# Kernel tuning notes

Hardware: AMD Instinct MI355X
Metric: run time of the kernel (lower is better)

Reference implementation:

```python
import jax, jax.numpy as jnp
import numpy as np

GROUPS = [[0, 1, 2, 3, 4], [5, 7, 9], [6, 8, 10], [11, 13, 15], [12, 14, 16]]
G = len(GROUPS)
BN_EPS = 1e-5


def _fc_edges(n):
    r = np.repeat(np.arange(n), n)
    c = np.tile(np.arange(n), n)
    m = r != c
    return jnp.asarray(r[m]), jnp.asarray(c[m])


ROW, COL = _fc_edges(G)  # [E], E = G*(G-1) = 20


def _bn(x, scale, bias, mean, var):
    # inference-mode batchnorm over last dim
    return (x - mean) * (scale * jax.lax.rsqrt(var + BN_EPS)) + bias


def setup_inputs() -> dict:
    key = jax.random.key(0)
    ks = jax.random.split(key, 12)
    B, K, C, Ci = 4096, 17, 256, 64
    inp = {
        "x_bk_c": jax.random.normal(ks[0], (B * K, C), jnp.float32),
        "W_down": jax.random.normal(ks[1], (C, Ci), jnp.float32) * 0.05,
        "b_down": jax.random.normal(ks[2], (Ci,), jnp.float32) * 0.05,
        "bn1_scale": jax.random.uniform(ks[3], (Ci,), jnp.float32, 0.5, 1.5),
        "bn1_bias": jax.random.normal(ks[4], (Ci,), jnp.float32) * 0.1,
        "bn1_mean": jax.random.normal(ks[5], (Ci,), jnp.float32) * 0.1,
        "bn1_var": jax.random.uniform(ks[6], (Ci,), jnp.float32, 0.5, 1.5),
        "W_conv": jax.random.normal(ks[7], (Ci, 2 * Ci), jnp.float32) * 0.05,  # 1x1 conv, bias=False
        "bn2_scale": jax.random.uniform(ks[8], (Ci,), jnp.float32, 0.5, 1.5),
        "bn2_bias": jax.random.normal(ks[9], (Ci,), jnp.float32) * 0.1,
        "bn2_mean": jax.random.normal(ks[10], (Ci,), jnp.float32) * 0.1,
        "bn2_var": jax.random.uniform(ks[11], (Ci,), jnp.float32, 0.5, 1.5),
        "W_agg": jax.random.normal(jax.random.fold_in(key, 100), (Ci, C), jnp.float32) * 0.05,
        "b_agg": jax.random.normal(jax.random.fold_in(key, 101), (C,), jnp.float32) * 0.05,
        "B": B,
        "K": K,
    }
    return inp


def reference(x_bk_c, W_down, b_down, bn1_scale, bn1_bias, bn1_mean, bn1_var,
              W_conv, bn2_scale, bn2_bias, bn2_mean, bn2_var, W_agg, b_agg, B, K):
    C = x_bk_c.shape[-1]
    # down-projection + BN + SiLU
    xd = jax.nn.silu(_bn(x_bk_c @ W_down + b_down, bn1_scale, bn1_bias, bn1_mean, bn1_var))
    xd = xd.reshape(B, K, -1)  # [B, K, Ci]
    # per-group mean pooling (static small loop over 5 groups)
    means = jnp.stack([xd[:, g, :].mean(axis=1) for g in GROUPS], axis=1)  # [B, G, Ci]
    # EdgeConv over fully-connected group graph
    x_i = means[:, ROW, :]                                   # [B, E, Ci]
    x_j = means[:, COL, :]
    ef = jnp.concatenate([x_i, x_j - x_i], axis=-1)          # [B, E, 2Ci]
    pe = jax.nn.silu(_bn(ef @ W_conv.T, bn2_scale, bn2_bias, bn2_mean, bn2_var))  # [B, E, Ci]
    agg = jnp.zeros_like(means).at[:, ROW, :].add(pe)        # scatter-add over target nodes
    # per-group attention scores in C_in
    att = jax.nn.sigmoid(agg @ W_agg + b_agg)                # [B, G, C]
    # average group scores over each keypoint's memberships
    M = np.zeros((K, G), np.float32)
    for gi, g in enumerate(GROUPS):
        for kp in g:
            M[kp, gi] += 1.0
    Mj = jnp.asarray(M)
    cnt = Mj.sum(axis=1, keepdims=True)                      # [K, 1]
    ssum = jnp.einsum('kg,bgc->bkc', Mj, att)                # [B, K, C]
    safe = jnp.where(cnt > 0, cnt, 1.0)
    final = jnp.where(cnt > 0, ssum / safe, 1.0)             # ungrouped kps -> 1.0
    return (x_bk_c.reshape(B, K, C) * final).reshape(B * K, C)
```

## Files before the change

kernel.cpp:

```cpp
#include <hip/hip_runtime.h>

typedef float  v4f    __attribute__((ext_vector_type(4)));
typedef float  f32x4  __attribute__((ext_vector_type(4)));
typedef short  bf16x8 __attribute__((ext_vector_type(8)));

namespace {
constexpr int XBSTR = 264;
constexpr int XDT   = 24;
constexpr int MWC   = 129;
constexpr int ATS   = 258;
constexpr int MSTR  = 72;
constexpr int FRAG_SLOTS = 5120;

__device__ __forceinline__ float fsilu(float v){ return v/(1.f+__expf(-v)); }
__device__ __forceinline__ float fsigm(float v){ return 1.f/(1.f+__expf(-v)); }

__device__ __forceinline__ unsigned f2bf2(float a, float b){
  unsigned r;
  asm("v_cvt_pk_bf16_f32 %0, %1, %2" : "=v"(r) : "v"(a), "v"(b));
  return r;
}
__device__ __forceinline__ short f2bf(float f){
  unsigned u = __builtin_bit_cast(unsigned, f);
  return (short)((u + 0x7FFFu + ((u>>16)&1u)) >> 16);
}
__device__ __forceinline__ float bf2f(short s){
  unsigned u = ((unsigned)(unsigned short)s) << 16;
  return __builtin_bit_cast(float, u);
}

template<bool USE_WS>
__device__ __forceinline__ bf16x8 get_bd(const bf16x8* wsf, const float* Wd,
                                         int nt, int ks, int l){
  if constexpr (USE_WS) return wsf[(nt*8 + ks)*64 + l];
  bf16x8 f;
  #pragma unroll
  for (int j = 0; j < 8; ++j) f[j] = f2bf(Wd[(ks*32 + (l>>4)*8 + j)*64 + nt*16 + (l&15)]);
  return f;
}
template<bool USE_WS>
__device__ __forceinline__ bf16x8 get_bc(const bf16x8* wsf, const float* Wc,
                                         int nt, int ks, int l){
  if constexpr (USE_WS) return wsf[2048 + (nt*2 + ks)*64 + l];
  const int col = nt*16 + (l&15), cw = col>>6, co = col&63;
  bf16x8 f;
  #pragma unroll
  for (int j = 0; j < 8; ++j) f[j] = f2bf(Wc[co*128 + cw*64 + ks*32 + (l>>4)*8 + j]);
  return f;
}
template<bool USE_WS>
__device__ __forceinline__ bf16x8 get_ba(const bf16x8* wsf, const float* Wa,
                                         int nt, int ks, int l){
  if constexpr (USE_WS) return wsf[3072 + (nt*2 + ks)*64 + l];
  const int col = nt*16 + (l&15);
  bf16x8 f;
  #pragma unroll
  for (int j = 0; j < 8; ++j) f[j] = f2bf(Wa[(ks*32 + (l>>4)*8 + j)*256 + col]);
  return f;
}
}

__global__ __launch_bounds__(256)
void pack_frags(const float* __restrict__ Wd, const float* __restrict__ Wc,
                const float* __restrict__ Wa, bf16x8* __restrict__ wsf)
{
  const int e  = blockIdx.x*256 + threadIdx.x;
  const int l  = e & 63;
  const int fi = e >> 6;
  bf16x8 f;
  if (fi < 32) {
    const int nt = fi >> 3, ks = fi & 7;
    #pragma unroll
    for (int j = 0; j < 8; ++j) f[j] = f2bf(Wd[(ks*32 + (l>>4)*8 + j)*64 + nt*16 + (l&15)]);
  } else if (fi < 48) {
    const int idx = fi - 32, nt = idx >> 1, ks = idx & 1;
    const int col = nt*16 + (l&15), cw = col>>6, co = col&63;
    #pragma unroll
    for (int j = 0; j < 8; ++j) f[j] = f2bf(Wc[co*128 + cw*64 + ks*32 + (l>>4)*8 + j]);
  } else {
    const int idx = fi - 48, nt = idx >> 1, ks = idx & 1;
    const int col = nt*16 + (l&15);
    #pragma unroll
    for (int j = 0; j < 8; ++j) f[j] = f2bf(Wa[(ks*32 + (l>>4)*8 + j)*256 + col]);
  }
  wsf[e] = f;
}

template<bool USE_WS>
__global__ __launch_bounds__(256, 8)
void fused_gnn_v9(const float* __restrict__ x,
                  const float* __restrict__ Wd, const float* __restrict__ bd,
                  const float* __restrict__ bn1s, const float* __restrict__ bn1b,
                  const float* __restrict__ bn1m, const float* __restrict__ bn1v,
                  const float* __restrict__ Wc,
                  const float* __restrict__ bn2s, const float* __restrict__ bn2b,
                  const float* __restrict__ bn2m, const float* __restrict__ bn2v,
                  const float* __restrict__ Wa, const float* __restrict__ ba,
                  const bf16x8* __restrict__ wsf,
                  float* __restrict__ out)
{
  __shared__ short xbf[18*XBSTR];
  __shared__ __align__(16) char uni_raw[3072];
  __shared__ float mw[5*MWC];
  __shared__ short mbf[16*MSTR];
  __shared__ short abf[16*MSTR];

  short* xdT = (short*)uni_raw;
  short* att = (short*)uni_raw;

  const int tid  = threadIdx.x;
  const int l    = tid & 63;
  const int wv   = tid >> 6;
  const int arow = l & 15;
  const int ak8  = (l >> 4) * 8;
  const int b    = blockIdx.x;
  const int colA = wv*16 + arow;

  const float a1r = bn1s[colA] * rsqrtf(bn1v[colA] + 1e-5f);
  const float b1r = (bd[colA] - bn1m[colA])*a1r + bn1b[colA];
  const float a2r = bn2s[l] * rsqrtf(bn2v[l] + 1e-5f);
  const float b2r = bn2b[l] - bn2m[l]*a2r;

  {
    const v4f* x4 = (const v4f*)(x + (size_t)b * 4352);
    #pragma unroll
    for (int i = 0; i < 5; ++i) {
      const int idx = i*256 + tid;
      if (idx < 1088) {
        const v4f v = x4[idx];
        const int r = idx >> 6, c4 = (idx & 63) * 4;
        uint2 u; u.x = f2bf2(v.x, v.y); u.y = f2bf2(v.z, v.w);
        *(uint2*)&xbf[r*XBSTR + c4] = u;
      }
    }
  }
  __syncthreads();

  {
    f32x4 acc0 = {0.f,0.f,0.f,0.f};
    f32x4 acc1 = {0.f,0.f,0.f,0.f};
    const int rowT = (arow == 0) ? 16 : 17;
    #pragma unroll
    for (int h = 0; h < 2; ++h) {
      bf16x8 Bd[4];
      #pragma unroll
      for (int k4 = 0; k4 < 4; ++k4) Bd[k4] = get_bd<USE_WS>(wsf, Wd, wv, h*4 + k4, l);
      #pragma unroll
      for (int k4 = 0; k4 < 4; ++k4) {
        const int ks = h*4 + k4;
        bf16x8 a0 = *(const bf16x8*)&xbf[arow*XBSTR + ks*32 + ak8];
        acc0 = __builtin_amdgcn_mfma_f32_16x16x32_bf16(a0, Bd[k4], acc0, 0, 0, 0);
        bf16x8 a1 = *(const bf16x8*)&xbf[rowT*XBSTR + ks*32 + ak8];
        acc1 = __builtin_amdgcn_mfma_f32_16x16x32_bf16(a1, Bd[k4], acc1, 0, 0, 0);
      }
    }
    const float s0 = fsilu(acc0[0]*a1r + b1r);
    const float s1 = fsilu(acc0[1]*a1r + b1r);
    const float s2 = fsilu(acc0[2]*a1r + b1r);
    const float s3 = fsilu(acc0[3]*a1r + b1r);
    uint2 u; u.x = f2bf2(s0, s1); u.y = f2bf2(s2, s3);
    *(uint2*)&xdT[colA*XDT + (l>>4)*4] = u;
    if ((l >> 4) == 0)
      xdT[colA*XDT + 16] = f2bf(fsilu(acc1[0]*a1r + b1r));
  }
  __syncthreads();

  {
    const bf16x8 rA = *(const bf16x8*)&xdT[l*XDT];
    const bf16x8 rB = *(const bf16x8*)&xdT[l*XDT + 8];
    const float x16 = bf2f(xdT[l*XDT + 16]);
    float xv[16];
    #pragma unroll
    for (int k = 0; k < 8; ++k) { xv[k] = bf2f(rA[k]); xv[k+8] = bf2f(rB[k]); }
    const float m0 = (xv[0]+xv[1]+xv[2]+xv[3]+xv[4])*0.2f;
    const float m1 = (xv[5]+xv[7]+xv[9])*(1.f/3.f);
    const float m2 = (xv[6]+xv[8]+xv[10])*(1.f/3.f);
    const float m3 = (xv[11]+xv[13]+xv[15])*(1.f/3.f);
    const float m4 = (xv[12]+xv[14]+x16)*(1.f/3.f);
    unsigned p01 = f2bf2(m0, m1);
    unsigned p23 = f2bf2(m2, m3);
    mbf[0*MSTR + l] = (short)(p01 & 0xFFFFu);
    mbf[1*MSTR + l] = (short)(p01 >> 16);
    mbf[2*MSTR + l] = (short)(p23 & 0xFFFFu);
    mbf[3*MSTR + l] = (short)(p23 >> 16);
    mbf[4*MSTR + l] = f2bf(m4);
  }

  {
    bf16x8 am[2];
    #pragma unroll
    for (int ks = 0; ks < 2; ++ks)
      am[ks] = *(const bf16x8*)&mbf[arow*MSTR + ks*32 + ak8];
    #pragma unroll
    for (int t = 0; t < 2; ++t) {
      const int nt = wv*2 + t;
      f32x4 acc = {0.f,0.f,0.f,0.f};
      #pragma unroll
      for (int ks = 0; ks < 2; ++ks)
        acc = __builtin_amdgcn_mfma_f32_16x16x32_bf16(
                am[ks], get_bc<USE_WS>(wsf, Wc, nt, ks, l), acc, 0, 0, 0);
      #pragma unroll
      for (int j = 0; j < 4; ++j) {
        const int g = (l>>4)*4 + j;
        if (g < 5) mw[g*MWC + nt*16 + arow] = acc[j];
      }
    }
  }
  __syncthreads();

  {
    float m2c[5];
    #pragma unroll
    for (int cc = 0; cc < 5; ++cc) m2c[cc] = mw[cc*MWC + 64 + l];
    #pragma unroll
    for (int g = 0; g < 5; ++g) {
      const float bse = mw[g*MWC + l] - m2c[g];
      float s = 0.f;
      #pragma unroll
      for (int cc = 0; cc < 5; ++cc) {
        if (cc != g) s += fsilu((bse + m2c[cc])*a2r + b2r);
      }
      abf[g*MSTR + l] = f2bf(s);
    }
  }

  {
    bf16x8 ae[2];
    #pragma unroll
    for (int ks = 0; ks < 2; ++ks)
      ae[ks] = *(const bf16x8*)&abf[arow*MSTR + ks*32 + ak8];
    #pragma unroll
    for (int t = 0; t < 4; ++t) {
      const int nt = wv*4 + t;
      const int colE = nt*16 + arow;
      f32x4 acc = {0.f,0.f,0.f,0.f};
      #pragma unroll
      for (int ks = 0; ks < 2; ++ks)
        acc = __builtin_amdgcn_mfma_f32_16x16x32_bf16(
                ae[ks], get_ba<USE_WS>(wsf, Wa, nt, ks, l), acc, 0, 0, 0);
      const float bav = ba[colE];
      #pragma unroll
      for (int j = 0; j < 4; ++j) {
        const int g = (l>>4)*4 + j;
        if (g < 5) att[g*ATS + colE] = f2bf(fsigm(acc[j] + bav));
      }
    }
  }
  __syncthreads();

  {
    const int c = tid;
    float a5[5];
    #pragma unroll
    for (int g = 0; g < 5; ++g) a5[g] = bf2f(att[g*ATS + c]);
    float* og = out + (size_t)b*4352 + c;
    constexpr int GOF[17] = {0,0,0,0,0,1,2,1,2,1,2,3,4,3,4,3,4};
    #pragma unroll
    for (int k = 0; k < 17; ++k)
      og[k*256] = bf2f(xbf[k*XBSTR + c]) * a5[GOF[k]];
  }
}

extern "C" void kernel_launch(void* const* d_in, const int* in_sizes, int n_in,
                              void* d_out, int out_size, void* d_ws, size_t ws_size,
                              hipStream_t stream) {
    (void)n_in; (void)out_size;
    const float* x   = (const float*)d_in[0];
    const float* Wd  = (const float*)d_in[1];
    const float* bd  = (const float*)d_in[2];
    const float* s1  = (const float*)d_in[3];
    const float* b1  = (const float*)d_in[4];
    const float* m1  = (const float*)d_in[5];
    const float* v1  = (const float*)d_in[6];
    const float* Wc  = (const float*)d_in[7];
    const float* s2  = (const float*)d_in[8];
    const float* b2  = (const float*)d_in[9];
    const float* m2  = (const float*)d_in[10];
    const float* v2  = (const float*)d_in[11];
    const float* Wa  = (const float*)d_in[12];
    const float* ba  = (const float*)d_in[13];

    const int Btot = in_sizes[0] / (17 * 256);
    bf16x8* wsf = (bf16x8*)d_ws;

    if (ws_size >= (size_t)FRAG_SLOTS * 16) {
        pack_frags<<<FRAG_SLOTS/256, 256, 0, stream>>>(Wd, Wc, Wa, wsf);
        fused_gnn_v9<true><<<Btot, 256, 0, stream>>>(
            x, Wd, bd, s1, b1, m1, v1, Wc, s2, b2, m2, v2, Wa, ba,
            wsf, (float*)d_out);
    } else {
        fused_gnn_v9<false><<<Btot, 256, 0, stream>>>(
            x, Wd, bd, s1, b1, m1, v1, Wc, s2, b2, m2, v2, Wa, ba,
            wsf, (float*)d_out);
    }
}
```

Baseline: 46.92 us.

## Process one batch item per wavefront, removing block barriers and x staging in LDS

Each wavefront now handles a whole batch item (4 items per block) instead of four waves sharing one item. x is loaded straight into registers as bf16 MFMA fragments rather than staged through shared memory, group means are reduced with cross-lane shuffles, and all __syncthreads are removed because each wave uses private LDS slices. This targets barrier stalls and LDS traffic. In exchange each wave does four times the MFMA and weight-fragment loads, register pressure goes up (launch bounds drop to 4), the grid assumes B is divisible by 4, and output is rebuilt from bf16-rounded x except for row 16.

```diff
diff --git a/kernel.cpp b/kernel.cpp
--- a/kernel.cpp
+++ b/kernel.cpp
@@ -1,15 +1,14 @@
 #include <hip/hip_runtime.h>
 
-typedef float  v4f    __attribute__((ext_vector_type(4)));
-typedef float  f32x4  __attribute__((ext_vector_type(4)));
-typedef short  bf16x8 __attribute__((ext_vector_type(8)));
+typedef float    v4f    __attribute__((ext_vector_type(4)));
+typedef float    f32x4  __attribute__((ext_vector_type(4)));
+typedef short    bf16x8 __attribute__((ext_vector_type(8)));
+typedef unsigned u32x4  __attribute__((ext_vector_type(4)));
 
 namespace {
-constexpr int XBSTR = 264;
-constexpr int XDT   = 24;
-constexpr int MWC   = 129;
-constexpr int ATS   = 258;
-constexpr int MSTR  = 72;
+constexpr int MSTR = 72;
+constexpr int MWC  = 129;
+constexpr int ATS  = 264;
 constexpr int FRAG_SLOTS = 5120;
 
 __device__ __forceinline__ float fsilu(float v){ return v/(1.f+__expf(-v)); }
@@ -27,6 +26,14 @@
 __device__ __forceinline__ float bf2f(short s){
   unsigned u = ((unsigned)(unsigned short)s) << 16;
   return __builtin_bit_cast(float, u);
+}
+__device__ __forceinline__ bf16x8 pack4(unsigned u0, unsigned u1, unsigned u2, unsigned u3){
+  u32x4 u = {u0, u1, u2, u3};
+  return __builtin_bit_cast(bf16x8, u);
+}
+__device__ __forceinline__ bf16x8 cvt8(v4f lo, v4f hi){
+  return pack4(f2bf2(lo.x, lo.y), f2bf2(lo.z, lo.w),
+               f2bf2(hi.x, hi.y), f2bf2(hi.z, hi.w));
 }
 
 template<bool USE_WS>
@@ -87,177 +94,192 @@
 }
 
 template<bool USE_WS>
-__global__ __launch_bounds__(256, 8)
-void fused_gnn_v9(const float* __restrict__ x,
-                  const float* __restrict__ Wd, const float* __restrict__ bd,
-                  const float* __restrict__ bn1s, const float* __restrict__ bn1b,
-                  const float* __restrict__ bn1m, const float* __restrict__ bn1v,
-                  const float* __restrict__ Wc,
-                  const float* __restrict__ bn2s, const float* __restrict__ bn2b,
-                  const float* __restrict__ bn2m, const float* __restrict__ bn2v,
-                  const float* __restrict__ Wa, const float* __restrict__ ba,
-                  const bf16x8* __restrict__ wsf,
-                  float* __restrict__ out)
+__global__ __launch_bounds__(256, 4)
+void fused_gnn_v19(const float* __restrict__ x,
+                   const float* __restrict__ Wd, const float* __restrict__ bd,
+                   const float* __restrict__ bn1s, const float* __restrict__ bn1b,
+                   const float* __restrict__ bn1m, const float* __restrict__ bn1v,
+                   const float* __restrict__ Wc,
+                   const float* __restrict__ bn2s, const float* __restrict__ bn2b,
+                   const float* __restrict__ bn2m, const float* __restrict__ bn2v,
+                   const float* __restrict__ Wa, const float* __restrict__ ba,
+                   const bf16x8* __restrict__ wsf,
+                   float* __restrict__ out)
 {
-  __shared__ short xbf[18*XBSTR];
-  __shared__ __align__(16) char uni_raw[3072];
-  __shared__ float mw[5*MWC];
-  __shared__ short mbf[16*MSTR];
-  __shared__ short abf[16*MSTR];
-
-  short* xdT = (short*)uni_raw;
-  short* att = (short*)uni_raw;
+  __shared__ short mbfs[4][21*MSTR];
+  __shared__ float mws [4][5*MWC];
+  __shared__ short atts[4][5*ATS];
 
   const int tid  = threadIdx.x;
   const int l    = tid & 63;
   const int wv   = tid >> 6;
+  short* mbf = mbfs[wv];
+  short* abf = mbfs[wv] + 5*MSTR;
+  float* mw  = mws[wv];
+  short* att = atts[wv];
+
   const int arow = l & 15;
-  const int ak8  = (l >> 4) * 8;
-  const int b    = blockIdx.x;
-  const int colA = wv*16 + arow;
-
-  const float a1r = bn1s[colA] * rsqrtf(bn1v[colA] + 1e-5f);
-  const float b1r = (bd[colA] - bn1m[colA])*a1r + bn1b[colA];
-  const float a2r = bn2s[l] * rsqrtf(bn2v[l] + 1e-5f);
+  const int q4   = l >> 4;
+  const int ak8  = q4 * 8;
+  const int b    = blockIdx.x*4 + wv;
+  const float* xb = x + (size_t)b * 4352;
+
+  float a1c0, a1c1, a1c2, a1c3, b1c0, b1c1, b1c2, b1c3;
+  {
+    const int c0 = 0*16+arow, c1 = 1*16+arow, c2 = 2*16+arow, c3 = 3*16+arow;
+    a1c0 = bn1s[c0]*rsqrtf(bn1v[c0]+1e-5f); b1c0 = (bd[c0]-bn1m[c0])*a1c0 + bn1b[c0];
+    a1c1 = bn1s[c1]*rsqrtf(bn1v[c1]+1e-5f); b1c1 = (bd[c1]-bn1m[c1])*a1c1 + bn1b[c1];
+    a1c2 = bn1s[c2]*rsqrtf(bn1v[c2]+1e-5f); b1c2 = (bd[c2]-bn1m[c2])*a1c2 + bn1b[c2];
+    a1c3 = bn1s[c3]*rsqrtf(bn1v[c3]+1e-5f); b1c3 = (bd[c3]-bn1m[c3])*a1c3 + bn1b[c3];
+  }
+  const float a2r = bn2s[l]*rsqrtf(bn2v[l]+1e-5f);
   const float b2r = bn2b[l] - bn2m[l]*a2r;
 
-  {
-    const v4f* x4 = (const v4f*)(x + (size_t)b * 4352);
-    #pragma unroll
-    for (int i = 0; i < 5; ++i) {
-      const int idx = i*256 + tid;
-      if (idx < 1088) {
-        const v4f v = x4[idx];
-        const int r = idx >> 6, c4 = (idx & 63) * 4;
-        uint2 u; u.x = f2bf2(v.x, v.y); u.y = f2bf2(v.z, v.w);
-        *(uint2*)&xbf[r*XBSTR + c4] = u;
-      }
-    }
-  }
-  __syncthreads();
-
-  {
+  bf16x8 xf[8];
+  bf16x8 xt[8];
+  {
+    const int rowT = (arow == 0) ? 16 : 0;
+    #pragma unroll
+    for (int ks = 0; ks < 8; ++ks) {
+      v4f lo = *(const v4f*)(xb + arow*256 + ks*32 + ak8);
+      v4f hi = *(const v4f*)(xb + arow*256 + ks*32 + ak8 + 4);
+      xf[ks] = cvt8(lo, hi);
+      v4f tl = *(const v4f*)(xb + rowT*256 + ks*32 + ak8);
+      v4f th = *(const v4f*)(xb + rowT*256 + ks*32 + ak8 + 4);
+      xt[ks] = cvt8(tl, th);
+    }
+  }
+
+  #pragma unroll
+  for (int nt = 0; nt < 4; ++nt) {
+    const float a1v = (nt==0)?a1c0:(nt==1)?a1c1:(nt==2)?a1c2:a1c3;
+    const float b1v = (nt==0)?b1c0:(nt==1)?b1c1:(nt==2)?b1c2:b1c3;
     f32x4 acc0 = {0.f,0.f,0.f,0.f};
     f32x4 acc1 = {0.f,0.f,0.f,0.f};
-    const int rowT = (arow == 0) ? 16 : 17;
     #pragma unroll
     for (int h = 0; h < 2; ++h) {
       bf16x8 Bd[4];
       #pragma unroll
-      for (int k4 = 0; k4 < 4; ++k4) Bd[k4] = get_bd<USE_WS>(wsf, Wd, wv, h*4 + k4, l);
+      for (int k4 = 0; k4 < 4; ++k4) Bd[k4] = get_bd<USE_WS>(wsf, Wd, nt, h*4 + k4, l);
       #pragma unroll
       for (int k4 = 0; k4 < 4; ++k4) {
         const int ks = h*4 + k4;
-        bf16x8 a0 = *(const bf16x8*)&xbf[arow*XBSTR + ks*32 + ak8];
-        acc0 = __builtin_amdgcn_mfma_f32_16x16x32_bf16(a0, Bd[k4], acc0, 0, 0, 0);
-        bf16x8 a1 = *(const bf16x8*)&xbf[rowT*XBSTR + ks*32 + ak8];
-        acc1 = __builtin_amdgcn_mfma_f32_16x16x32_bf16(a1, Bd[k4], acc1, 0, 0, 0);
+        acc0 = __builtin_amdgcn_mfma_f32_16x16x32_bf16(xf[ks], Bd[k4], acc0, 0, 0, 0);
+        acc1 = __builtin_amdgcn_mfma_f32_16x16x32_bf16(xt[ks], Bd[k4], acc1, 0, 0, 0);
       }
     }
-    const float s0 = fsilu(acc0[0]*a1r + b1r);
-    const float s1 = fsilu(acc0[1]*a1r + b1r);
-    const float s2 = fsilu(acc0[2]*a1r + b1r);
-    const float s3 = fsilu(acc0[3]*a1r + b1r);
-    uint2 u; u.x = f2bf2(s0, s1); u.y = f2bf2(s2, s3);
-    *(uint2*)&xdT[colA*XDT + (l>>4)*4] = u;
-    if ((l >> 4) == 0)
-      xdT[colA*XDT + 16] = f2bf(fsilu(acc1[0]*a1r + b1r));
-  }
-  __syncthreads();
-
-  {
-    const bf16x8 rA = *(const bf16x8*)&xdT[l*XDT];
-    const bf16x8 rB = *(const bf16x8*)&xdT[l*XDT + 8];
-    const float x16 = bf2f(xdT[l*XDT + 16]);
-    float xv[16];
-    #pragma unroll
-    for (int k = 0; k < 8; ++k) { xv[k] = bf2f(rA[k]); xv[k+8] = bf2f(rB[k]); }
-    const float m0 = (xv[0]+xv[1]+xv[2]+xv[3]+xv[4])*0.2f;
-    const float m1 = (xv[5]+xv[7]+xv[9])*(1.f/3.f);
-    const float m2 = (xv[6]+xv[8]+xv[10])*(1.f/3.f);
-    const float m3 = (xv[11]+xv[13]+xv[15])*(1.f/3.f);
-    const float m4 = (xv[12]+xv[14]+x16)*(1.f/3.f);
-    unsigned p01 = f2bf2(m0, m1);
-    unsigned p23 = f2bf2(m2, m3);
-    mbf[0*MSTR + l] = (short)(p01 & 0xFFFFu);
-    mbf[1*MSTR + l] = (short)(p01 >> 16);
-    mbf[2*MSTR + l] = (short)(p23 & 0xFFFFu);
-    mbf[3*MSTR + l] = (short)(p23 >> 16);
-    mbf[4*MSTR + l] = f2bf(m4);
-  }
-
-  {
-    bf16x8 am[2];
-    #pragma unroll
-    for (int ks = 0; ks < 2; ++ks)
-      am[ks] = *(const bf16x8*)&mbf[arow*MSTR + ks*32 + ak8];
-    #pragma unroll
-    for (int t = 0; t < 2; ++t) {
-      const int nt = wv*2 + t;
+    const float s0 = fsilu(acc0[0]*a1v + b1v);
+    const float s1 = fsilu(acc0[1]*a1v + b1v);
+    const float s2 = fsilu(acc0[2]*a1v + b1v);
+    const float s3 = fsilu(acc0[3]*a1v + b1v);
+    const float st = fsilu(acc1[0]*a1v + b1v);
+    float p0 = 0.f, p1 = 0.f, p2 = 0.f, p3 = 0.f, p4 = 0.f;
+    if (q4 == 0)      { p0 = s0+s1+s2+s3; p4 = st; }
+    else if (q4 == 1) { p0 = s0; p1 = s1+s3; p2 = s2; }
+    else if (q4 == 2) { p2 = s0+s2; p1 = s1; p3 = s3; }
+    else              { p4 = s0+s2; p3 = s1+s3; }
+    p0 += __shfl_xor(p0, 16); p0 += __shfl_xor(p0, 32);
+    p1 += __shfl_xor(p1, 16); p1 += __shfl_xor(p1, 32);
+    p2 += __shfl_xor(p2, 16); p2 += __shfl_xor(p2, 32);
+    p3 += __shfl_xor(p3, 16); p3 += __shfl_xor(p3, 32);
+    p4 += __shfl_xor(p4, 16); p4 += __shfl_xor(p4, 32);
+    if (q4 == 0) {
+      const int col = nt*16 + arow;
+      mbf[0*MSTR + col] = f2bf(p0 * 0.2f);
+      mbf[1*MSTR + col] = f2bf(p1 * (1.f/3.f));
+      mbf[2*MSTR + col] = f2bf(p2 * (1.f/3.f));
+      mbf[3*MSTR + col] = f2bf(p3 * (1.f/3.f));
+      mbf[4*MSTR + col] = f2bf(p4 * (1.f/3.f));
+    }
+  }
+
+  {
+    const bf16x8 am0 = *(const bf16x8*)&mbf[arow*MSTR + 0*32 + ak8];
+    const bf16x8 am1 = *(const bf16x8*)&mbf[arow*MSTR + 1*32 + ak8];
+    #pragma unroll
+    for (int nt = 0; nt < 8; ++nt) {
       f32x4 acc = {0.f,0.f,0.f,0.f};
+      acc = __builtin_amdgcn_mfma_f32_16x16x32_bf16(am0, get_bc<USE_WS>(wsf, Wc, nt, 0, l), acc, 0, 0, 0);
+      acc = __builtin_amdgcn_mfma_f32_16x16x32_bf16(am1, get_bc<USE_WS>(wsf, Wc, nt, 1, l), acc, 0, 0, 0);
+      if (q4 == 0) {
+        #pragma unroll
+        for (int j = 0; j < 4; ++j) mw[j*MWC + nt*16 + arow] = acc[j];
+      } else if (q4 == 1) {
+        mw[4*MWC + nt*16 + arow] = acc[0];
+      }
+    }
+  }
+
+  {
+    const float c0 = mw[0*MWC + 64 + l];
+    const float c1 = mw[1*MWC + 64 + l];
+    const float c2 = mw[2*MWC + 64 + l];
+    const float c3 = mw[3*MWC + 64 + l];
+    const float c4 = mw[4*MWC + 64 + l];
+    auto doG = [&](int g, float m2g){
+      const float bse = mw[g*MWC + l] - m2g;
+      float s = 0.f;
+      if (g != 0) s += fsilu((bse + c0)*a2r + b2r);
+      if (g != 1) s += fsilu((bse + c1)*a2r + b2r);
+      if (g != 2) s += fsilu((bse + c2)*a2r + b2r);
+      if (g != 3) s += fsilu((bse + c3)*a2r + b2r);
+      if (g != 4) s += fsilu((bse + c4)*a2r + b2r);
+      abf[g*MSTR + l] = f2bf(s);
+    };
+    doG(0, c0); doG(1, c1); doG(2, c2); doG(3, c3); doG(4, c4);
+  }
+
+  {
+    const bf16x8 ae0 = *(const bf16x8*)&abf[arow*MSTR + 0*32 + ak8];
+    const bf16x8 ae1 = *(const bf16x8*)&abf[arow*MSTR + 1*32 + ak8];
+    #pragma unroll
+    for (int nt = 0; nt < 16; ++nt) {
+      f32x4 acc = {0.f,0.f,0.f,0.f};
+      acc = __builtin_amdgcn_mfma_f32_16x16x32_bf16(ae0, get_ba<USE_WS>(wsf, Wa, nt, 0, l), acc, 0, 0, 0);
+      acc = __builtin_amdgcn_mfma_f32_16x16x32_bf16(ae1, get_ba<USE_WS>(wsf, Wa, nt, 1, l), acc, 0, 0, 0);
+      const int colE = nt*16 + arow;
+      if (q4 == 0) {
+        const float bav = ba[colE];
+        #pragma unroll
+        for (int j = 0; j < 4; ++j)
+          att[j*ATS + colE] = f2bf(fsigm(acc[j] + bav));
+      } else if (q4 == 1) {
+        att[4*ATS + colE] = f2bf(fsigm(acc[0] + ba[colE]));
+      }
+    }
+  }
+
+  {
+    float* og = out + (size_t)b * 4352;
+    const int g = (arow < 5) ? 0 : (arow < 11 ? ((arow & 1) ? 1 : 2)
+                                              : ((arow & 1) ? 3 : 4));
+    #pragma unroll
+    for (int ks = 0; ks < 8; ++ks) {
+      const bf16x8 a8 = *(const bf16x8*)&att[g*ATS + ks*32 + ak8];
+      const bf16x8 xk = xf[ks];
+      v4f o0, o1;
+      o0.x = bf2f(xk[0])*bf2f(a8[0]); o0.y = bf2f(xk[1])*bf2f(a8[1]);
+      o0.z = bf2f(xk[2])*bf2f(a8[2]); o0.w = bf2f(xk[3])*bf2f(a8[3]);
+      o1.x = bf2f(xk[4])*bf2f(a8[4]); o1.y = bf2f(xk[5])*bf2f(a8[5]);
+      o1.z = bf2f(xk[6])*bf2f(a8[6]); o1.w = bf2f(xk[7])*bf2f(a8[7]);
+      *(v4f*)(og + arow*256 + ks*32 + ak8)     = o0;
+      *(v4f*)(og + arow*256 + ks*32 + ak8 + 4) = o1;
+    }
+    if (arow == 0) {
       #pragma unroll
-      for (int ks = 0; ks < 2; ++ks)
-        acc = __builtin_amdgcn_mfma_f32_16x16x32_bf16(
-                am[ks], get_bc<USE_WS>(wsf, Wc, nt, ks, l), acc, 0, 0, 0);
-      #pragma unroll
-      for (int j = 0; j < 4; ++j) {
-        const int g = (l>>4)*4 + j;
-        if (g < 5) mw[g*MWC + nt*16 + arow] = acc[j];
+      for (int ks = 0; ks < 8; ++ks) {
+        const v4f lo = *(const v4f*)(xb + 16*256 + ks*32 + ak8);
+        const v4f hi = *(const v4f*)(xb + 16*256 + ks*32 + ak8 + 4);
+        const bf16x8 a8 = *(const bf16x8*)&att[4*ATS + ks*32 + ak8];
+        v4f o0, o1;
+        o0.x = lo.x*bf2f(a8[0]); o0.y = lo.y*bf2f(a8[1]);
+        o0.z = lo.z*bf2f(a8[2]); o0.w = lo.w*bf2f(a8[3]);
+        o1.x = hi.x*bf2f(a8[4]); o1.y = hi.y*bf2f(a8[5]);
+        o1.z = hi.z*bf2f(a8[6]); o1.w = hi.w*bf2f(a8[7]);
+        *(v4f*)(og + 16*256 + ks*32 + ak8)     = o0;
+        *(v4f*)(og + 16*256 + ks*32 + ak8 + 4) = o1;
       }
     }
-  }
-  __syncthreads();
-
-  {
-    float m2c[5];
-    #pragma unroll
-    for (int cc = 0; cc < 5; ++cc) m2c[cc] = mw[cc*MWC + 64 + l];
-    #pragma unroll
-    for (int g = 0; g < 5; ++g) {
-      const float bse = mw[g*MWC + l] - m2c[g];
-      float s = 0.f;
-      #pragma unroll
-      for (int cc = 0; cc < 5; ++cc) {
-        if (cc != g) s += fsilu((bse + m2c[cc])*a2r + b2r);
-      }
-      abf[g*MSTR + l] = f2bf(s);
-    }
-  }
-
-  {
-    bf16x8 ae[2];
-    #pragma unroll
-    for (int ks = 0; ks < 2; ++ks)
-      ae[ks] = *(const bf16x8*)&abf[arow*MSTR + ks*32 + ak8];
-    #pragma unroll
-    for (int t = 0; t < 4; ++t) {
-      const int nt = wv*4 + t;
-      const int colE = nt*16 + arow;
-      f32x4 acc = {0.f,0.f,0.f,0.f};
-      #pragma unroll
-      for (int ks = 0; ks < 2; ++ks)
-        acc = __builtin_amdgcn_mfma_f32_16x16x32_bf16(
-                ae[ks], get_ba<USE_WS>(wsf, Wa, nt, ks, l), acc, 0, 0, 0);
-      const float bav = ba[colE];
-      #pragma unroll
-      for (int j = 0; j < 4; ++j) {
-        const int g = (l>>4)*4 + j;
-        if (g < 5) att[g*ATS + colE] = f2bf(fsigm(acc[j] + bav));
-      }
-    }
-  }
-  __syncthreads();
-
-  {
-    const int c = tid;
-    float a5[5];
-    #pragma unroll
-    for (int g = 0; g < 5; ++g) a5[g] = bf2f(att[g*ATS + c]);
-    float* og = out + (size_t)b*4352 + c;
-    constexpr int GOF[17] = {0,0,0,0,0,1,2,1,2,1,2,3,4,3,4,3,4};
-    #pragma unroll
-    for (int k = 0; k < 17; ++k)
-      og[k*256] = bf2f(xbf[k*XBSTR + c]) * a5[GOF[k]];
   }
 }
 
@@ -281,15 +303,16 @@
     const float* ba  = (const float*)d_in[13];
 
     const int Btot = in_sizes[0] / (17 * 256);
+    const int GRID = Btot / 4;
     bf16x8* wsf = (bf16x8*)d_ws;
 
     if (ws_size >= (size_t)FRAG_SLOTS * 16) {
         pack_frags<<<FRAG_SLOTS/256, 256, 0, stream>>>(Wd, Wc, Wa, wsf);
-        fused_gnn_v9<true><<<Btot, 256, 0, stream>>>(
+        fused_gnn_v19<true><<<GRID, 256, 0, stream>>>(
             x, Wd, bd, s1, b1, m1, v1, Wc, s2, b2, m2, v2, Wa, ba,
             wsf, (float*)d_out);
     } else {
-        fused_gnn_v9<false><<<Btot, 256, 0, stream>>>(
+        fused_gnn_v19<false><<<GRID, 256, 0, stream>>>(
             x, Wd, bd, s1, b1, m1, v1, Wc, s2, b2, m2, v2, Wa, ba,
             wsf, (float*)d_out);
     }
```

Measured after the change: 65.84 us. +40.3%, slower.
